# Performance work log

Measured on AMD Instinct MI355X. Metric: run time of the kernel, lower is better.

The kernel has to match this reference:

```python
import jax, jax.numpy as jnp
import numpy as np
from jax import lax

B, T, K, HID, NCLS = 32, 2048, 17, 64, 10
DILATIONS = (1, 1, 2)
RESIDUAL = (False, True, True)
TK = 3  # temporal kernel
BN_EPS = 1e-5
LN_EPS = 1e-5

COCO_EDGES = [(0,1),(0,2),(1,3),(2,4),(5,6),(5,7),(7,9),(6,8),(8,10),(5,11),(6,12),(11,13),(13,15),(12,14),(14,16)]

def build_skeleton_adj(num_kpts=K):
    adj = np.eye(num_kpts, dtype=np.float32)
    for i, j in COCO_EDGES:
        adj[i, j] = 1.0
        adj[j, i] = 1.0
    adj = adj + np.eye(num_kpts, dtype=np.float32)
    deg = adj.sum(axis=1, keepdims=True)
    deg[deg == 0] = 1.0
    return adj / deg

def setup_inputs() -> dict:
    key = jax.random.key(0)
    ks = jax.random.split(key, 8)
    kpts = jax.random.normal(ks[0], (B, T, K, 3), dtype=jnp.float32)
    adj = jnp.asarray(build_skeleton_adj(K))
    gcn_w0 = jax.random.normal(ks[1], (3, HID), dtype=jnp.float32) * (1.0 / np.sqrt(3))
    gcn_w1 = jax.random.normal(ks[2], (HID, HID), dtype=jnp.float32) * (1.0 / np.sqrt(HID))
    gcn_w2 = jax.random.normal(ks[3], (HID, HID), dtype=jnp.float32) * (1.0 / np.sqrt(HID))
    tcn_w = jax.random.normal(ks[4], (3, HID, HID, TK, 1), dtype=jnp.float32) * (1.0 / np.sqrt(HID * TK))
    bn_scale = 1.0 + 0.1 * jax.random.normal(ks[5], (3, HID), dtype=jnp.float32)
    bn_bias = 0.1 * jax.random.normal(ks[6], (3, HID), dtype=jnp.float32)
    bn_mean = 0.1 * jax.random.normal(ks[7], (3, HID), dtype=jnp.float32)
    bn_var = 0.5 + jax.random.uniform(jax.random.fold_in(key, 7), (3, HID), dtype=jnp.float32)
    ln_scale = jnp.ones((HID,), dtype=jnp.float32)
    ln_bias = jnp.zeros((HID,), dtype=jnp.float32)
    fc_w = jax.random.normal(jax.random.fold_in(key, 8), (HID, NCLS), dtype=jnp.float32) * (1.0 / np.sqrt(HID))
    fc_b = jnp.zeros((NCLS,), dtype=jnp.float32)
    return dict(kpts=kpts, adj=adj, gcn_w0=gcn_w0, gcn_w1=gcn_w1, gcn_w2=gcn_w2,
                tcn_w=tcn_w, bn_scale=bn_scale, bn_bias=bn_bias, bn_mean=bn_mean,
                bn_var=bn_var, ln_scale=ln_scale, ln_bias=ln_bias, fc_w=fc_w, fc_b=fc_b)

def _stgn_block(x, adj, gw, tw, bs, bb, bm, bv, dilation, residual):
    # x: [B, C_in, T, K]
    y = jnp.einsum('bctk,kv->bctv', x, adj)          # graph conv over keypoints
    y = jnp.einsum('bitk,io->botk', y, gw)           # channel mixing (intended GCN weight)
    pad = (TK - 1) * dilation // 2
    y = lax.conv_general_dilated(y, tw, window_strides=(1, 1),
                                 padding=[(pad, pad), (0, 0)],
                                 rhs_dilation=(dilation, 1),
                                 dimension_numbers=('NCHW', 'OIHW', 'NCHW'))
    inv = (bs / jnp.sqrt(bv + BN_EPS))[None, :, None, None]
    y = y * inv + (bb - bs * bm / jnp.sqrt(bv + BN_EPS))[None, :, None, None]
    y = jax.nn.relu(y)
    if residual:
        y = y + x
    return y

def reference(kpts, adj, gcn_w0, gcn_w1, gcn_w2, tcn_w, bn_scale, bn_bias, bn_mean,
              bn_var, ln_scale, ln_bias, fc_w, fc_b):
    x = jnp.transpose(kpts, (0, 3, 1, 2))  # [B, 3, T, K]
    gws = (gcn_w0, gcn_w1, gcn_w2)
    for i in range(3):
        x = _stgn_block(x, adj, gws[i], tcn_w[i], bn_scale[i], bn_bias[i],
                        bn_mean[i], bn_var[i], DILATIONS[i], RESIDUAL[i])
    feat = x.mean(axis=(2, 3))  # [B, HID] temporal/spatial mean pool
    mu = feat.mean(axis=-1, keepdims=True)
    var = feat.var(axis=-1, keepdims=True)
    feat = (feat - mu) / jnp.sqrt(var + LN_EPS) * ln_scale + ln_bias
    return feat @ fc_w + fc_b  # [B, NCLS]
```

## Files before the change

kernel.cpp:

```cpp
#include <hip/hip_runtime.h>
#include <hip/hip_fp16.h>
#include <math.h>

#define T_DIM 2048
#define TP_DIM 2056
#define K_DIM 17
#define HID   64
#define B_DIM 32

typedef short s16x8 __attribute__((ext_vector_type(8)));
typedef unsigned u32x2 __attribute__((ext_vector_type(2)));
typedef float f32x4 __attribute__((ext_vector_type(4)));
typedef _Float16 f16x2 __attribute__((ext_vector_type(2)));

__device__ __forceinline__ unsigned pkh(float lo, float hi) {
    return __builtin_bit_cast(unsigned, __builtin_amdgcn_cvt_pkrtz(lo, hi));
}
__device__ __forceinline__ f16x2 u2h(unsigned v) {
    return __builtin_bit_cast(f16x2, v);
}
__device__ __forceinline__ unsigned h2u(f16x2 v) {
    return __builtin_bit_cast(unsigned, v);
}
__device__ __forceinline__ short f2h(float f) {
    _Float16 h = (_Float16)f;
    return __builtin_bit_cast(short, h);
}

static constexpr int NBR_PTR[18] = {0,3,6,9,11,13,17,21,24,27,29,31,34,37,40,43,45,47};
static constexpr int NBR_K[47] = {
    0,1,2,  0,1,3,  0,2,4,  1,3,  2,4,
    5,6,7,11,  5,6,8,12,  5,7,9,  6,8,10,  7,9,  8,10,
    5,11,13,  6,12,14,  11,13,15,  12,14,16,  13,15,  14,16 };
__device__ const int d_NBR_PTR[18] = {0,3,6,9,11,13,17,21,24,27,29,31,34,37,40,43,45,47};
__device__ const int d_NBR_K[47] = {
    0,1,2,  0,1,3,  0,2,4,  1,3,  2,4,
    5,6,7,11,  5,6,8,12,  5,7,9,  6,8,10,  7,9,  8,10,
    5,11,13,  6,12,14,  11,13,15,  12,14,16,  13,15,  14,16 };

__global__ void fold_weights_kernel(
    const float* __restrict__ gw0, const float* __restrict__ gw1,
    const float* __restrict__ gw2, const float* __restrict__ tcn,
    const float* __restrict__ bns, const float* __restrict__ bnb,
    const float* __restrict__ bnm, const float* __restrict__ bnv,
    short* __restrict__ effT0, short* __restrict__ effT12,
    float* __restrict__ bnc)
{
    int tid = blockIdx.x * blockDim.x + threadIdx.x;
    int stride = gridDim.x * blockDim.x;
    for (int idx = tid; idx < 2048; idx += stride) {
        int o = idx >> 5, k = idx & 31, dt = k >> 3, cin = k & 7;
        float s = 0.f;
        if (dt < 3 && cin < 3)
            for (int m = 0; m < 64; m++)
                s += gw0[cin * 64 + m] * tcn[(o * 64 + m) * 3 + dt];
        effT0[idx] = f2h(s);
    }
    for (int idx = tid; idx < 24576; idx += stride) {
        int blk = idx / 12288;
        int r = idx - blk * 12288;
        int o = r / 192, k = r - o * 192, dt = k >> 6, c = k & 63;
        const float* gw = blk ? gw2 : gw1;
        const float* tw = tcn + (size_t)(blk + 1) * 64 * 64 * 3;
        float s = 0.f;
        for (int m = 0; m < 64; m++)
            s += gw[c * 64 + m] * tw[(o * 64 + m) * 3 + dt];
        effT12[idx] = f2h(s);
    }
    for (int i = tid; i < 192; i += stride) {
        float inv = bns[i] * rsqrtf(bnv[i] + 1e-5f);
        bnc[i] = inv;
        bnc[192 + i] = bnb[i] - bnm[i] * inv;
    }
}

__global__ __launch_bounds__(256) void premix_kernel(
    const float* __restrict__ x, const float* __restrict__ adj,
    float* __restrict__ xg, int cb)
{
    const int idx = blockIdx.x * 256 + threadIdx.x;
    const int total = cb * TP_DIM * K_DIM;
    if (idx >= total) return;
    const int b = idx / (TP_DIM * K_DIM);
    const int rem = idx - b * (TP_DIM * K_DIM);
    const int tp = rem / K_DIM, j = rem - tp * K_DIM;
    const int t = tp - 4;
    float a0 = 0.f, a1 = 0.f, a2 = 0.f;
    if (t >= 0 && t < T_DIM) {
        const float* xp = x + ((size_t)b * T_DIM + t) * 51;
        const int p0 = d_NBR_PTR[j], p1 = d_NBR_PTR[j + 1];
        for (int e = p0; e < p1; e++) {
            int k = d_NBR_K[e];
            float w = adj[k * 17 + j];
            a0 += w * xp[k * 3 + 0];
            a1 += w * xp[k * 3 + 1];
            a2 += w * xp[k * 3 + 2];
        }
    }
    float* op = xg + ((size_t)b * TP_DIM + tp) * 52 + j * 3;
    op[0] = a0; op[1] = a1; op[2] = a2;
}

__global__ __launch_bounds__(256, 4) void stgcn_mono_kernel(
    const float* __restrict__ xg, const float* __restrict__ adj,
    const short* __restrict__ effT0, const short* __restrict__ effT12,
    const float* __restrict__ bnc, float* __restrict__ part, int b0)
{
    __shared__ unsigned adj_h[289];
    __shared__ __align__(16) float xtg[16 * 52];
    __shared__ __align__(16) short ybuf[238 * 72];

    float* prm = (float*)xtg;
    float* pr1 = (float*)xtg + 512;

    const int tid = threadIdx.x;
    const int b = blockIdx.y;
    const int t0 = blockIdx.x * 8;
    const int lane = tid & 63, wave = tid >> 6;
    const int col = lane & 15, kgrp = lane >> 4;

    for (int i = tid; i < 289; i += 256) {
        float w = adj[i];
        adj_h[i] = pkh(w, w);
    }
    {
        const float4* src = (const float4*)(xg + ((size_t)b * TP_DIM + t0) * 52);
        float4* dst = (float4*)xtg;
        for (int i = tid; i < 208; i += 256) dst[i] = src[i];
    }
    s16x8 af1 = *(const s16x8*)(effT0 + (wave * 16 + col) * 32 + kgrp * 8);
    s16x8 af2[6];
    #pragma unroll
    for (int kk = 0; kk < 6; kk++)
        af2[kk] = *(const s16x8*)(effT12 +
            (wave * 16 + col) * 192 + kk * 32 + kgrp * 8);
    __syncthreads();

    {
        f32x4 inv4 = *(const f32x4*)&bnc[wave * 16 + kgrp * 4];
        f32x4 sh4  = *(const f32x4*)&bnc[192 + wave * 16 + kgrp * 4];
        for (int tile = 0; tile < 15; tile++) {
            const int r = tile * 16 + col;
            const int me = r < 238 ? r : 237;
            const int s = (me * 241) >> 12;
            const int j = me - s * 17;
            int4 bz = {0, 0, 0, 0};
            if (kgrp < 3) {
                const float* xp = &xtg[(s + kgrp) * 52 + j * 3];
                bz.x = (int)pkh(xp[0], xp[1]);
                bz.y = (int)pkh(xp[2], 0.f);
            }
            s16x8 bfr = __builtin_bit_cast(s16x8, bz);
            f32x4 acc = __builtin_amdgcn_mfma_f32_16x16x32_f16(
                af1, bfr, (f32x4){0.f, 0.f, 0.f, 0.f}, 0, 0, 0);
            const int t = t0 - 3 + s;
            const bool valid = (t >= 0) && (t < T_DIM);
            if (r < 238) {
                float v0 = valid ? fmaxf(acc[0] * inv4[0] + sh4[0], 0.f) : 0.f;
                float v1 = valid ? fmaxf(acc[1] * inv4[1] + sh4[1], 0.f) : 0.f;
                float v2 = valid ? fmaxf(acc[2] * inv4[2] + sh4[2], 0.f) : 0.f;
                float v3 = valid ? fmaxf(acc[3] * inv4[3] + sh4[3], 0.f) : 0.f;
                u32x2 st; st[0] = pkh(v0, v1); st[1] = pkh(v2, v3);
                *(u32x2*)&ybuf[r * 72 + wave * 16 + kgrp * 4] = st;
            }
        }
    }
    __syncthreads();

    const int tl0 = tid >> 5, oq = tid & 31, o0 = oq * 2;
    unsigned rv[2][17];
    #pragma unroll
    for (int v = 0; v < 17; v++)
        rv[0][v] = *(const unsigned*)&ybuf[((tl0 + 1) * 17 + v) * 72 + o0];
    if (tid < 128) {
        #pragma unroll
        for (int v = 0; v < 17; v++)
            rv[1][v] = *(const unsigned*)&ybuf[((tl0 + 9) * 17 + v) * 72 + o0];
    }

    f32x4 accA[7];
    #pragma unroll
    for (int t2 = 0; t2 < 7; t2++) accA[t2] = (f32x4){0.f, 0.f, 0.f, 0.f};
    #pragma unroll
    for (int kk = 0; kk < 6; kk++) {
        #pragma unroll
        for (int t2 = 0; t2 < 7; t2++) {
            const int r = t2 * 16 + col;
            s16x8 bfr = *(const s16x8*)&ybuf[
                (r + 17 * (kk >> 1)) * 72 + (kk & 1) * 32 + kgrp * 8];
            accA[t2] = __builtin_amdgcn_mfma_f32_16x16x32_f16(
                af2[kk], bfr, accA[t2], 0, 0, 0);
        }
    }
    __syncthreads();

    #pragma unroll
    for (int t2 = 0; t2 < 7; t2++) {
        const int r = t2 * 16 + col;
        u32x2 st;
        st[0] = pkh(accA[t2][0], accA[t2][1]);
        st[1] = pkh(accA[t2][2], accA[t2][3]);
        *(u32x2*)&ybuf[r * 72 + wave * 16 + kgrp * 4] = st;
    }
    f32x4 accB[6];
    #pragma unroll
    for (int t2 = 0; t2 < 6; t2++) accB[t2] = (f32x4){0.f, 0.f, 0.f, 0.f};
    #pragma unroll
    for (int kk = 0; kk < 6; kk++) {
        #pragma unroll
        for (int t2 = 0; t2 < 6; t2++) {
            const int r = (t2 + 7) * 16 + col;
            const int me = r < 204 ? r : 203;
            s16x8 bfr = *(const s16x8*)&ybuf[
                (me + 17 * (kk >> 1)) * 72 + (kk & 1) * 32 + kgrp * 8];
            accB[t2] = __builtin_amdgcn_mfma_f32_16x16x32_f16(
                af2[kk], bfr, accB[t2], 0, 0, 0);
        }
    }
    __syncthreads();

    #pragma unroll
    for (int t2 = 0; t2 < 6; t2++) {
        const int r = (t2 + 7) * 16 + col;
        if (r < 204) {
            u32x2 st;
            st[0] = pkh(accB[t2][0], accB[t2][1]);
            st[1] = pkh(accB[t2][2], accB[t2][3]);
            *(u32x2*)&ybuf[r * 72 + wave * 16 + kgrp * 4] = st;
        }
    }
    __syncthreads();

    {
        const f16x2 inv2 = u2h(pkh(bnc[64 + o0], bnc[64 + o0 + 1]));
        const f16x2 sh2  = u2h(pkh(bnc[256 + o0], bnc[256 + o0 + 1]));
        const f16x2 zero = u2h(0u);
        #pragma unroll
        for (int it = 0; it < 2; it++) {
            const int tl = tl0 + it * 8;
            if (it == 1 && tid >= 128) break;
            const int t = t0 - 2 + tl;
            const bool valid = (t >= 0) && (t < T_DIM);
            f16x2 zk[17];
            #pragma unroll
            for (int k = 0; k < 17; k++)
                zk[k] = u2h(*(const unsigned*)&ybuf[(tl * 17 + k) * 72 + o0]);
            f16x2 y2v[17];
            f16x2 pool = zero;
            #pragma unroll
            for (int v = 0; v < 17; v++) {
                f16x2 g = zero;
                #pragma unroll
                for (int e = NBR_PTR[v]; e < NBR_PTR[v + 1]; e++) {
                    int k = NBR_K[e];
                    g = u2h(adj_h[k * 17 + v]) * zk[k] + g;
                }
                f16x2 val = __builtin_elementwise_max(g * inv2 + sh2, zero);
                val = val + u2h(rv[it][v]);
                if (!valid) val = zero;
                y2v[v] = val;
                pool = pool + val;
            }
            if (tl >= 2 && tl <= 9) {
                prm[(tl - 2) * 64 + o0]     = (float)pool[0];
                prm[(tl - 2) * 64 + o0 + 1] = (float)pool[1];
            }
            #pragma unroll
            for (int j = 0; j < 17; j++) {
                f16x2 gg = zero;
                #pragma unroll
                for (int e = NBR_PTR[j]; e < NBR_PTR[j + 1]; e++) {
                    int k = NBR_K[e];
                    gg = u2h(adj_h[k * 17 + j]) * y2v[k] + gg;
                }
                *(unsigned*)&ybuf[(tl * 17 + j) * 72 + o0] = h2u(gg);
            }
        }
    }
    __syncthreads();

    {
        s16x8 af3[6];
        #pragma unroll
        for (int kk = 0; kk < 6; kk++)
            af3[kk] = *(const s16x8*)(effT12 + 12288 +
                (wave * 16 + col) * 192 + kk * 32 + kgrp * 8);
        const f32x4 inv4 = *(const f32x4*)&bnc[128 + wave * 16 + kgrp * 4];
        const f32x4 sh4  = *(const f32x4*)&bnc[320 + wave * 16 + kgrp * 4];
        float psum[4] = {0.f, 0.f, 0.f, 0.f};
        for (int t3 = 0; t3 < 9; t3++) {
            const int r = t3 * 16 + col;
            const int me = r < 136 ? r : 135;
            f32x4 acc = (f32x4){0.f, 0.f, 0.f, 0.f};
            #pragma unroll
            for (int kk = 0; kk < 6; kk++) {
                s16x8 bfr = *(const s16x8*)&ybuf[
                    (me + 34 * (kk >> 1)) * 72 + (kk & 1) * 32 + kgrp * 8];
                acc = __builtin_amdgcn_mfma_f32_16x16x32_f16(
                    af3[kk], bfr, acc, 0, 0, 0);
            }
            if (r < 136) {
                psum[0] += fmaxf(acc[0] * inv4[0] + sh4[0], 0.f);
                psum[1] += fmaxf(acc[1] * inv4[1] + sh4[1], 0.f);
                psum[2] += fmaxf(acc[2] * inv4[2] + sh4[2], 0.f);
                psum[3] += fmaxf(acc[3] * inv4[3] + sh4[3], 0.f);
            }
        }
        #pragma unroll
        for (int off = 1; off <= 8; off <<= 1) {
            psum[0] += __shfl_xor(psum[0], off);
            psum[1] += __shfl_xor(psum[1], off);
            psum[2] += __shfl_xor(psum[2], off);
            psum[3] += __shfl_xor(psum[3], off);
        }
        if (col == 0)
            *(f32x4*)&pr1[wave * 16 + kgrp * 4] =
                (f32x4){psum[0], psum[1], psum[2], psum[3]};
    }
    __syncthreads();
    if (tid < 64) {
        float s = pr1[tid];
        #pragma unroll
        for (int i = 0; i < 8; i++) s += prm[i * 64 + tid];
        part[((size_t)(b0 + b) * 256 + blockIdx.x) * 64 + tid] = s;
    }
}

__global__ __launch_bounds__(256) void finish_kernel(
    const float* __restrict__ part, const float* __restrict__ ln_s,
    const float* __restrict__ ln_b, const float* __restrict__ fc_w,
    const float* __restrict__ fc_b, float* __restrict__ out)
{
    __shared__ float red[4][64];
    __shared__ float ns[64];
    const int b = blockIdx.x;
    const int g = threadIdx.x >> 6, c = threadIdx.x & 63;
    float s = 0.f;
    for (int j = 0; j < 64; j++)
        s += part[((size_t)b * 256 + g * 64 + j) * 64 + c];
    red[g][c] = s;
    __syncthreads();
    if (threadIdx.x < 64) {
        float feat = (red[0][c] + red[1][c] + red[2][c] + red[3][c])
                   / (float)(T_DIM * K_DIM);
        float m = feat;
        #pragma unroll
        for (int off = 32; off > 0; off >>= 1) m += __shfl_down(m, off);
        m = __shfl(m, 0) / 64.f;
        float d = feat - m;
        float v = d * d;
        #pragma unroll
        for (int off = 32; off > 0; off >>= 1) v += __shfl_down(v, off);
        v = __shfl(v, 0) / 64.f;
        ns[c] = d * rsqrtf(v + 1e-5f) * ln_s[c] + ln_b[c];
    }
    __syncthreads();
    if (threadIdx.x < 10) {
        float o = fc_b[threadIdx.x];
        for (int i = 0; i < 64; i++) o += ns[i] * fc_w[i * 10 + threadIdx.x];
        out[b * 10 + threadIdx.x] = o;
    }
}

extern "C" void kernel_launch(void* const* d_in, const int* in_sizes, int n_in,
                              void* d_out, int out_size, void* d_ws, size_t ws_size,
                              hipStream_t stream)
{
    const float* kpts = (const float*)d_in[0];
    const float* adj  = (const float*)d_in[1];
    const float* gw0  = (const float*)d_in[2];
    const float* gw1  = (const float*)d_in[3];
    const float* gw2  = (const float*)d_in[4];
    const float* tcn  = (const float*)d_in[5];
    const float* bns  = (const float*)d_in[6];
    const float* bnb  = (const float*)d_in[7];
    const float* bnm  = (const float*)d_in[8];
    const float* bnv  = (const float*)d_in[9];
    const float* lns  = (const float*)d_in[10];
    const float* lnb  = (const float*)d_in[11];
    const float* fcw  = (const float*)d_in[12];
    const float* fcb  = (const float*)d_in[13];
    float* out = (float*)d_out;

    float* bnc  = (float*)d_ws;
    float* part = bnc + 384;
    short* effT0  = (short*)(part + (size_t)B_DIM * 256 * 64);
    short* effT12 = effT0 + 2048;
    float* xg = (float*)(effT12 + 24576);
    const size_t fixed_bytes = 384 * 4 + (size_t)B_DIM * 256 * 64 * 4
                             + 2048 * 2 + 24576 * 2;
    const size_t xg_per_b = (size_t)TP_DIM * 52 * 4;

    int cb = B_DIM;
    while (cb > 1 && fixed_bytes + (size_t)cb * xg_per_b > ws_size) cb >>= 1;

    fold_weights_kernel<<<64, 256, 0, stream>>>(gw0, gw1, gw2, tcn,
                                                bns, bnb, bnm, bnv,
                                                effT0, effT12, bnc);

    const int pm_blocks = (cb * TP_DIM * K_DIM + 255) / 256;
    for (int b0 = 0; b0 < B_DIM; b0 += cb) {
        premix_kernel<<<pm_blocks, 256, 0, stream>>>(
            kpts + (size_t)b0 * T_DIM * K_DIM * 3, adj, xg, cb);
        stgcn_mono_kernel<<<dim3(T_DIM / 8, cb), 256, 0, stream>>>(
            xg, adj, effT0, effT12, bnc, part, b0);
    }

    finish_kernel<<<B_DIM, 256, 0, stream>>>(part, lns, lnb, fcw, fcb, out);
}
```

Measured before the change: 235.7 us.

## Fuse adjacency premix into the main ST-GCN kernel and drop intermediate buffer

Removes the separate premix kernel that wrote a padded graph-mixed input buffer to global memory. Each block of the main kernel now loads its 16-frame raw keypoint window, including zero padding at the sequence edges, into shared memory reused from ybuf, and applies the sparse adjacency mixing itself before the existing MFMA pipeline. This eliminates one kernel launch, the global write and read of the xg buffer, and the batch chunking loop. In exchange it adds an extra barrier and some scalar work per block, and halo frames are recomputed by neighbouring blocks. The fold-weights grid size is also changed.

```diff
diff --git a/kernel.cpp b/kernel.cpp
--- a/kernel.cpp
+++ b/kernel.cpp
@@ -3,7 +3,6 @@
 #include <math.h>
 
 #define T_DIM 2048
-#define TP_DIM 2056
 #define K_DIM 17
 #define HID   64
 #define B_DIM 32
@@ -74,42 +73,17 @@
     }
 }
 
-__global__ __launch_bounds__(256) void premix_kernel(
+__global__ __launch_bounds__(256, 4) void stgcn_mono_kernel(
     const float* __restrict__ x, const float* __restrict__ adj,
-    float* __restrict__ xg, int cb)
-{
-    const int idx = blockIdx.x * 256 + threadIdx.x;
-    const int total = cb * TP_DIM * K_DIM;
-    if (idx >= total) return;
-    const int b = idx / (TP_DIM * K_DIM);
-    const int rem = idx - b * (TP_DIM * K_DIM);
-    const int tp = rem / K_DIM, j = rem - tp * K_DIM;
-    const int t = tp - 4;
-    float a0 = 0.f, a1 = 0.f, a2 = 0.f;
-    if (t >= 0 && t < T_DIM) {
-        const float* xp = x + ((size_t)b * T_DIM + t) * 51;
-        const int p0 = d_NBR_PTR[j], p1 = d_NBR_PTR[j + 1];
-        for (int e = p0; e < p1; e++) {
-            int k = d_NBR_K[e];
-            float w = adj[k * 17 + j];
-            a0 += w * xp[k * 3 + 0];
-            a1 += w * xp[k * 3 + 1];
-            a2 += w * xp[k * 3 + 2];
-        }
-    }
-    float* op = xg + ((size_t)b * TP_DIM + tp) * 52 + j * 3;
-    op[0] = a0; op[1] = a1; op[2] = a2;
-}
-
-__global__ __launch_bounds__(256, 4) void stgcn_mono_kernel(
-    const float* __restrict__ xg, const float* __restrict__ adj,
     const short* __restrict__ effT0, const short* __restrict__ effT12,
-    const float* __restrict__ bnc, float* __restrict__ part, int b0)
+    const float* __restrict__ bnc, float* __restrict__ part)
 {
     __shared__ unsigned adj_h[289];
+    __shared__ float adj_s[289];
     __shared__ __align__(16) float xtg[16 * 52];
     __shared__ __align__(16) short ybuf[238 * 72];
 
+    float* xs  = (float*)ybuf;
     float* prm = (float*)xtg;
     float* pr1 = (float*)xtg + 512;
 
@@ -122,11 +96,16 @@
     for (int i = tid; i < 289; i += 256) {
         float w = adj[i];
         adj_h[i] = pkh(w, w);
+        adj_s[i] = w;
     }
     {
-        const float4* src = (const float4*)(xg + ((size_t)b * TP_DIM + t0) * 52);
-        float4* dst = (float4*)xtg;
-        for (int i = tid; i < 208; i += 256) dst[i] = src[i];
+        const int tbase = t0 - 4;
+        const int lo_i = (tbase < 0) ? (-tbase) * 51 : 0;
+        const int hr = T_DIM - tbase;
+        const int hi_i = (hr >= 16) ? 816 : (hr < 0 ? 0 : hr * 51);
+        const float* xb = x + ((size_t)b * T_DIM + tbase) * 51;
+        for (int i = tid; i < 816; i += 256)
+            xs[i] = (i >= lo_i && i < hi_i) ? xb[i] : 0.f;
     }
     s16x8 af1 = *(const s16x8*)(effT0 + (wave * 16 + col) * 32 + kgrp * 8);
     s16x8 af2[6];
@@ -134,6 +113,25 @@
     for (int kk = 0; kk < 6; kk++)
         af2[kk] = *(const s16x8*)(effT12 +
             (wave * 16 + col) * 192 + kk * 32 + kgrp * 8);
+    __syncthreads();
+
+    for (int it = tid; it < 272; it += 256) {
+        const int row = (it * 241) >> 12;
+        const int j = it - row * 17;
+        const float* xp = &xs[row * 51];
+        float a0 = 0.f, a1 = 0.f, a2 = 0.f;
+        const int p0 = d_NBR_PTR[j], p1 = d_NBR_PTR[j + 1];
+        for (int e = p0; e < p1; e++) {
+            int k = d_NBR_K[e];
+            float w = adj_s[k * 17 + j];
+            a0 += w * xp[k * 3 + 0];
+            a1 += w * xp[k * 3 + 1];
+            a2 += w * xp[k * 3 + 2];
+        }
+        xtg[row * 52 + j * 3 + 0] = a0;
+        xtg[row * 52 + j * 3 + 1] = a1;
+        xtg[row * 52 + j * 3 + 2] = a2;
+    }
     __syncthreads();
 
     {
@@ -322,7 +320,7 @@
         float s = pr1[tid];
         #pragma unroll
         for (int i = 0; i < 8; i++) s += prm[i * 64 + tid];
-        part[((size_t)(b0 + b) * 256 + blockIdx.x) * 64 + tid] = s;
+        part[((size_t)b * 256 + blockIdx.x) * 64 + tid] = s;
     }
 }
 
@@ -386,25 +384,13 @@
     float* part = bnc + 384;
     short* effT0  = (short*)(part + (size_t)B_DIM * 256 * 64);
     short* effT12 = effT0 + 2048;
-    float* xg = (float*)(effT12 + 24576);
-    const size_t fixed_bytes = 384 * 4 + (size_t)B_DIM * 256 * 64 * 4
-                             + 2048 * 2 + 24576 * 2;
-    const size_t xg_per_b = (size_t)TP_DIM * 52 * 4;
-
-    int cb = B_DIM;
-    while (cb > 1 && fixed_bytes + (size_t)cb * xg_per_b > ws_size) cb >>= 1;
-
-    fold_weights_kernel<<<64, 256, 0, stream>>>(gw0, gw1, gw2, tcn,
+
+    fold_weights_kernel<<<96, 256, 0, stream>>>(gw0, gw1, gw2, tcn,
                                                 bns, bnb, bnm, bnv,
                                                 effT0, effT12, bnc);
 
-    const int pm_blocks = (cb * TP_DIM * K_DIM + 255) / 256;
-    for (int b0 = 0; b0 < B_DIM; b0 += cb) {
-        premix_kernel<<<pm_blocks, 256, 0, stream>>>(
-            kpts + (size_t)b0 * T_DIM * K_DIM * 3, adj, xg, cb);
-        stgcn_mono_kernel<<<dim3(T_DIM / 8, cb), 256, 0, stream>>>(
-            xg, adj, effT0, effT12, bnc, part, b0);
-    }
+    stgcn_mono_kernel<<<dim3(T_DIM / 8, B_DIM), 256, 0, stream>>>(
+        kpts, adj, effT0, effT12, bnc, part);
 
     finish_kernel<<<B_DIM, 256, 0, stream>>>(part, lns, lnb, fcw, fcb, out);
 }
```

Result: no change. 235.5 us (-0.1%).
